# Optimization experiments

Hardware: AMD Instinct MI355X
Metric: run time of the kernel (lower is better)

Reference implementation:

```python
import jax, jax.numpy as jnp
import numpy as np
import math

D_MODEL = 1024
NUM_HEADS = 16
HEAD_DIM = D_MODEL // NUM_HEADS
EPS = 1e-6
ROPE_BASE = 10000.0


def _rope_cos_sin(seq_len, dim, dtype):
    inv_freq = 1.0 / (ROPE_BASE ** (jnp.arange(0, dim, 2, dtype=jnp.float32) / dim))
    t = jnp.arange(seq_len, dtype=jnp.float32)
    freqs = jnp.outer(t, inv_freq)                 # [s, dim/2]
    emb = jnp.concatenate([freqs, freqs], axis=-1)  # [s, dim]
    return jnp.cos(emb).astype(dtype), jnp.sin(emb).astype(dtype)


def _rotate_half(x):
    x1, x2 = jnp.split(x, 2, axis=-1)
    return jnp.concatenate([-x2, x1], axis=-1)


def setup_inputs() -> dict:
    key = jax.random.key(0)
    k1, k2, k3 = jax.random.split(key, 3)
    b, s = 2, 2048
    x = jax.random.normal(k1, (b, s, D_MODEL), dtype=jnp.float32)
    norm_w = jnp.ones((D_MODEL,), dtype=jnp.float32)
    qkv_w = jax.random.normal(k2, (3 * D_MODEL, D_MODEL), dtype=jnp.float32) * (1.0 / math.sqrt(D_MODEL))
    qkv_b = jnp.zeros((3 * D_MODEL,), dtype=jnp.float32)
    proj_w = jax.random.normal(k3, (D_MODEL, D_MODEL), dtype=jnp.float32) * (1.0 / math.sqrt(D_MODEL))
    proj_b = jnp.zeros((D_MODEL,), dtype=jnp.float32)
    return {"x": x, "norm_w": norm_w, "qkv_w": qkv_w, "qkv_b": qkv_b,
            "proj_w": proj_w, "proj_b": proj_b}


def reference(x, norm_w, qkv_w, qkv_b, proj_w, proj_b):
    b, s, d = x.shape
    # RMSNorm (pre-LN)
    xn = x * jax.lax.rsqrt(jnp.mean(x * x, axis=-1, keepdims=True) + EPS) * norm_w
    # Fused QKV
    qkv = jnp.einsum('bsd,ed->bse', xn, qkv_w) + qkv_b
    q, k, v = jnp.split(qkv, 3, axis=-1)
    # [b, h, s, hd]
    def shape(t):
        return t.reshape(b, s, NUM_HEADS, HEAD_DIM).transpose(0, 2, 1, 3)
    q, k, v = shape(q), shape(k), shape(v)
    # RoPE on head_dim
    cos, sin = _rope_cos_sin(s, HEAD_DIM, x.dtype)  # [s, hd]
    q = q * cos + _rotate_half(q) * sin
    k = k * cos + _rotate_half(k) * sin
    # Naive causal attention
    scale = 1.0 / math.sqrt(HEAD_DIM)
    scores = jnp.einsum('bhqd,bhkd->bhqk', q, k) * scale
    causal = jnp.tril(jnp.ones((s, s), dtype=bool))
    scores = jnp.where(causal, scores, -jnp.inf)
    attn = jax.nn.softmax(scores, axis=-1)
    y = jnp.einsum('bhqk,bhkd->bhqd', attn, v)
    y = y.transpose(0, 2, 1, 3).reshape(b, s, d)
    return jnp.einsum('bsd,ed->bse', y, proj_w) + proj_b
```

## Files before the change

kernel.cpp:

```cpp
#include <hip/hip_runtime.h>
#include <cstdint>
#include <cstddef>

#define NB 2
#define NS 2048
#define ND 1024
#define NH 16
#define HD 64
#define ROWS 4096
#define E3 3072

using bf16 = __bf16;
typedef __attribute__((ext_vector_type(4))) __bf16 bf16x4;
typedef __attribute__((ext_vector_type(8))) __bf16 bf16x8;
typedef __attribute__((ext_vector_type(4))) float f32x4;

__device__ __forceinline__ f32x4 mfma16(bf16x8 a, bf16x8 b, f32x4 c) {
    return __builtin_amdgcn_mfma_f32_16x16x32_bf16(a, b, c, 0, 0, 0);
}

__device__ __forceinline__ void gll16(const bf16* src, bf16* lds) {
    __builtin_amdgcn_global_load_lds(
        (const __attribute__((address_space(1))) void*)src,
        (__attribute__((address_space(3))) void*)lds, 16, 0, 0);
}

__global__ __launch_bounds__(256) void prep(const float* __restrict__ qkv_w,
                                            const float* __restrict__ proj_w,
                                            const float* __restrict__ x,
                                            const float* __restrict__ norm_w,
                                            bf16* __restrict__ wq,
                                            bf16* __restrict__ xn,
                                            float4* __restrict__ tab) {
    __shared__ float wsum[4];
    int bid = blockIdx.x;
    int tid = threadIdx.x;
    if (bid < 4096) {
        const int n1 = E3 * ND;
        int i = (bid * 256 + tid) * 4;
        const float* src = (i < n1) ? (qkv_w + i) : (proj_w + (i - n1));
        float4 v = *(const float4*)src;
        bf16x4 o;
        o[0] = (bf16)v.x; o[1] = (bf16)v.y; o[2] = (bf16)v.z; o[3] = (bf16)v.w;
        *(bf16x4*)(wq + i) = o;
    } else if (bid < 8192) {
        int row = bid - 4096;
        const float* xr = x + (size_t)row * ND;
        float4 v = ((const float4*)xr)[tid];
        float ss = v.x*v.x + v.y*v.y + v.z*v.z + v.w*v.w;
        #pragma unroll
        for (int m = 32; m >= 1; m >>= 1) ss += __shfl_xor(ss, m);
        if ((tid & 63) == 0) wsum[tid >> 6] = ss;
        __syncthreads();
        float total = wsum[0] + wsum[1] + wsum[2] + wsum[3];
        float scale = rsqrtf(total * (1.0f / ND) + 1e-6f);
        float4 wv = ((const float4*)norm_w)[tid];
        bf16x4 o;
        o[0] = (bf16)(v.x * scale * wv.x);
        o[1] = (bf16)(v.y * scale * wv.y);
        o[2] = (bf16)(v.z * scale * wv.z);
        o[3] = (bf16)(v.w * scale * wv.w);
        ((bf16x4*)(xn + (size_t)row * ND))[tid] = o;
    } else {
        int idx = (bid - 8192) * 256 + tid;
        int s = idx >> 4, j = idx & 15;
        float f0 = powf(10000.0f, -(float)j * (1.0f / 32.0f));
        float f1 = powf(10000.0f, -(float)(j + 16) * (1.0f / 32.0f));
        float sn0, c0, sn1, c1;
        sincosf((float)s * f0, &sn0, &c0);
        sincosf((float)s * f1, &sn1, &c1);
        tab[idx] = make_float4(c0, sn0, c1, sn1);
    }
}

__global__ __launch_bounds__(256) void gemm_qkv_rope(const bf16* __restrict__ A,
                                                     const bf16* __restrict__ Bm,
                                                     const float* __restrict__ bias,
                                                     const float4* __restrict__ tab,
                                                     bf16* __restrict__ Qb,
                                                     bf16* __restrict__ Kb,
                                                     bf16* __restrict__ Vf) {
    const int K = ND;
    __shared__ bf16 smem[8192];
    bf16* Asm = smem;
    bf16* Bsm = smem + 4096;
    const int tid = threadIdx.x;
    const int wave = tid >> 6, lane = tid & 63;
    const int quad = lane >> 4, l15 = lane & 15;
    const int row0 = blockIdx.x * 128, col0 = blockIdx.y * 128;
    const int wr = (wave >> 1) * 64, wc = (wave & 1) * 64;
    const int srow = lane >> 2;
    const int scol = (lane & 3) * 8;

    f32x4 acc[4][4] = {};

    for (int k0 = 0; k0 < K; k0 += 32) {
        #pragma unroll
        for (int i = 0; i < 2; ++i) {
            int r = wave * 32 + i * 16;
            gll16(A + (size_t)(row0 + r + srow) * K + k0 + scol, Asm + r * 32);
            gll16(Bm + (size_t)(col0 + r + srow) * K + k0 + scol, Bsm + r * 32);
        }
        __syncthreads();
        bf16x8 af[4], bff[4];
        #pragma unroll
        for (int t = 0; t < 4; ++t) {
            af[t]  = *(const bf16x8*)(Asm + (wr + t * 16 + l15) * 32 + quad * 8);
            bff[t] = *(const bf16x8*)(Bsm + (wc + t * 16 + l15) * 32 + quad * 8);
        }
        #pragma unroll
        for (int mt = 0; mt < 4; ++mt)
            #pragma unroll
            for (int nt = 0; nt < 4; ++nt)
                acc[mt][nt] = mfma16(af[mt], bff[nt], acc[mt][nt]);
        __syncthreads();
    }

    float bb[4];
    #pragma unroll
    for (int nt = 0; nt < 4; ++nt) bb[nt] = bias[col0 + wc + nt * 16 + l15];

    const int region = col0 >> 10;
    if (region == 2) {
        const int cv = col0 - 2048 + wc;
        const int h = cv >> 6;
        const int b = row0 >> 11;
        const int sloc = row0 & (NS - 1);
        const int kg0 = (sloc + wr) >> 5;
        bf16* vh = Vf + (size_t)(b * NH + h) * 131072;
        #pragma unroll
        for (int Gw = 0; Gw < 2; ++Gw) {
            #pragma unroll
            for (int nt = 0; nt < 4; ++nt) {
                bf16x8 vf8;
                #pragma unroll
                for (int r = 0; r < 4; ++r) {
                    vf8[r]     = (bf16)(acc[2 * Gw][nt][r] + bb[nt]);
                    vf8[4 + r] = (bf16)(acc[2 * Gw + 1][nt][r] + bb[nt]);
                }
                *(bf16x8*)(vh + ((size_t)(kg0 + Gw) * 4 + nt) * 512 + lane * 8) = vf8;
            }
        }
    } else {
        const float scale = (region == 0) ? 0.125f : 1.0f;
        bf16* Ob = (region == 0) ? Qb : Kb;
        const int h = ((col0 + wc) & 1023) >> 6;
        bf16* ep = smem + wave * 2048;
        #pragma unroll
        for (int p = 0; p < 2; ++p) {
            #pragma unroll
            for (int mtl = 0; mtl < 2; ++mtl) {
                const int mt = p * 2 + mtl;
                #pragma unroll
                for (int r = 0; r < 4; ++r) {
                    int row = row0 + wr + mt * 16 + quad * 4 + r;
                    int s = row & (NS - 1);
                    float4 cs = tab[s * 16 + l15];
                    #pragma unroll
                    for (int nt = 0; nt < 4; ++nt) {
                        float v  = acc[mt][nt][r] + bb[nt];
                        float vp = acc[mt][nt ^ 2][r] + bb[nt ^ 2];
                        float cc = (nt & 1) ? cs.z : cs.x;
                        float ss = (nt & 1) ? cs.w : cs.y;
                        float res = (nt < 2) ? (v * cc - vp * ss) : (v * cc + vp * ss);
                        ep[(mtl * 16 + quad * 4 + r) * 64 + nt * 16 + l15] = (bf16)(res * scale);
                    }
                }
            }
            asm volatile("s_waitcnt lgkmcnt(0)" ::: "memory");
            const int rowp = row0 + wr + p * 32;
            const int b = rowp >> 11;
            const int s0p = rowp & (NS - 1);
            bf16* gbase = Ob + ((size_t)(b * NH + h) * NS + s0p + (lane >> 3)) * 64 + (lane & 7) * 8;
            const bf16* lbase = ep + (lane >> 3) * 64 + (lane & 7) * 8;
            #pragma unroll
            for (int i = 0; i < 4; ++i) {
                bf16x8 v8 = *(const bf16x8*)(lbase + i * 512);
                *(bf16x8*)(gbase + (size_t)i * 512) = v8;
            }
            asm volatile("s_waitcnt lgkmcnt(0)" ::: "memory");
        }
    }
}

__global__ __launch_bounds__(256) void gemm_proj(const bf16* __restrict__ A,
                                                 const bf16* __restrict__ Bm,
                                                 const float* __restrict__ bias,
                                                 float* __restrict__ C) {
    __shared__ bf16 Asm[128 * 32];
    __shared__ bf16 Bsm[64 * 32];
    const int tid = threadIdx.x;
    const int wave = tid >> 6, lane = tid & 63;
    const int quad = lane >> 4, l15 = lane & 15;
    const int row0 = blockIdx.x * 128, col0 = blockIdx.y * 64;
    const int wr = (wave >> 1) * 64, wc = (wave & 1) * 32;
    const int srow = lane >> 2;
    const int scol = (lane & 3) * 8;

    f32x4 acc[4][2] = {};

    for (int k0 = 0; k0 < ND; k0 += 32) {
        gll16(A + (size_t)(row0 + wave * 32 + srow) * ND + k0 + scol, Asm + (wave * 32) * 32);
        gll16(A + (size_t)(row0 + wave * 32 + 16 + srow) * ND + k0 + scol, Asm + (wave * 32 + 16) * 32);
        gll16(Bm + (size_t)(col0 + wave * 16 + srow) * ND + k0 + scol, Bsm + (wave * 16) * 32);
        __syncthreads();
        bf16x8 af[4], bff[2];
        #pragma unroll
        for (int t = 0; t < 4; ++t)
            af[t] = *(const bf16x8*)(Asm + (wr + t * 16 + l15) * 32 + quad * 8);
        #pragma unroll
        for (int t = 0; t < 2; ++t)
            bff[t] = *(const bf16x8*)(Bsm + (wc + t * 16 + l15) * 32 + quad * 8);
        #pragma unroll
        for (int mt = 0; mt < 4; ++mt)
            #pragma unroll
            for (int nt = 0; nt < 2; ++nt)
                acc[mt][nt] = mfma16(af[mt], bff[nt], acc[mt][nt]);
        __syncthreads();
    }

    #pragma unroll
    for (int nt = 0; nt < 2; ++nt) {
        int col = col0 + wc + nt * 16 + l15;
        float bv = bias[col];
        #pragma unroll
        for (int mt = 0; mt < 4; ++mt) {
            int row = row0 + wr + mt * 16 + quad * 4;
            #pragma unroll
            for (int r = 0; r < 4; ++r)
                C[(size_t)(row + r) * ND + col] = acc[mt][nt][r] + bv;
        }
    }
}

__global__ __launch_bounds__(256) void attn(const bf16* __restrict__ Q,
                                            const bf16* __restrict__ K,
                                            const bf16* __restrict__ Vf,
                                            bf16* __restrict__ Y) {
    __shared__ bf16 Ksm[2][8192];
    __shared__ bf16 Vsm[2][8192];
    int bid = blockIdx.x;
    int g = bid >> 5;
    int bh = bid & 31;
    int qt = (g < 8) ? (15 - g) : (g - 8);
    int tid = threadIdx.x;
    int wave = tid >> 6, lane = tid & 63;
    int quad = lane >> 4, l15 = lane & 15;
    int q0 = qt * 128 + wave * 32;
    const bf16* Qh = Q + (size_t)bh * NS * 64;
    const bf16* Kh = K + (size_t)bh * NS * 64;
    const float NEG_INF = -__builtin_inff();

    const int krow = wave * 8 + (lane >> 3);
    const int ksx  = (lane & 7) ^ (krow & 7);
    const bf16* sK = Kh + (size_t)krow * 64 + ksx * 8;
    const bf16* sV = Vf + (size_t)bh * 131072 + wave * 2048 + lane * 8;

    const bf16* pk0 = &Ksm[0][l15 * 64 + ((quad) ^ (l15 & 7)) * 8];
    const bf16* pk1 = &Ksm[0][l15 * 64 + ((4 + quad) ^ (l15 & 7)) * 8];
    const bf16* pvf = &Vsm[0][lane * 8];

    bf16x8 bq[2][2];
    #pragma unroll
    for (int t = 0; t < 2; ++t)
        #pragma unroll
        for (int hh = 0; hh < 2; ++hh)
            bq[t][hh] = *(const bf16x8*)(Qh + (size_t)(q0 + t * 16 + l15) * 64 + hh * 32 + quad * 8);

    f32x4 o[2][4] = {};
    float lsum[2] = {0.f, 0.f};

    auto stage = [&](int c, int par) {
        const int kb = c * 128;
        bf16* dK = &Ksm[par][wave * 512];
        bf16* dV = &Vsm[par][wave * 2048];
        #pragma unroll
        for (int i = 0; i < 4; ++i)
            gll16(sK + (size_t)(kb + i * 32) * 64, dK + i * 2048);
        #pragma unroll
        for (int nt = 0; nt < 4; ++nt)
            gll16(sV + (size_t)(kb >> 5) * 2048 + nt * 512, dV + nt * 512);
    };

    auto compute = [&](int cc, int par) {
        const int kb = cc * 128;
        const int pb = par * 8192;
        #pragma unroll
        for (int ksub = 0; ksub < 4; ++ksub) {
            const int kbs = kb + ksub * 32;
            if (kbs <= q0) {
                bf16x8 ak00 = *(const bf16x8*)(pk0 + pb + ksub * 2048);
                bf16x8 ak01 = *(const bf16x8*)(pk1 + pb + ksub * 2048);
                bf16x8 ak10 = *(const bf16x8*)(pk0 + pb + ksub * 2048 + 1024);
                bf16x8 ak11 = *(const bf16x8*)(pk1 + pb + ksub * 2048 + 1024);
                bf16x8 vf0 = *(const bf16x8*)(pvf + pb + ksub * 2048);
                bf16x8 vf1 = *(const bf16x8*)(pvf + pb + ksub * 2048 + 512);
                bf16x8 vf2 = *(const bf16x8*)(pvf + pb + ksub * 2048 + 1024);
                bf16x8 vf3 = *(const bf16x8*)(pvf + pb + ksub * 2048 + 1536);
                const bool masked = (kbs == q0);
                #pragma unroll
                for (int t = 0; t < 2; ++t) {
                    f32x4 sh0 = {}, sh1 = {};
                    sh0 = mfma16(ak00, bq[t][0], sh0);
                    sh0 = mfma16(ak01, bq[t][1], sh0);
                    sh1 = mfma16(ak10, bq[t][0], sh1);
                    sh1 = mfma16(ak11, bq[t][1], sh1);
                    if (masked) {
                        int qy = q0 + t * 16 + l15;
                        #pragma unroll
                        for (int r = 0; r < 4; ++r) {
                            if (kbs + quad * 4 + r > qy)      sh0[r] = NEG_INF;
                            if (kbs + 16 + quad * 4 + r > qy) sh1[r] = NEG_INF;
                        }
                    }
                    bf16x8 pa;
                    float ls = 0.f;
                    #pragma unroll
                    for (int j = 0; j < 4; ++j) {
                        float p0 = __expf(sh0[j]);
                        float p1 = __expf(sh1[j]);
                        ls += p0 + p1;
                        pa[j] = (bf16)p0;
                        pa[4 + j] = (bf16)p1;
                    }
                    lsum[t] += ls;
                    o[t][0] = mfma16(pa, vf0, o[t][0]);
                    o[t][1] = mfma16(pa, vf1, o[t][1]);
                    o[t][2] = mfma16(pa, vf2, o[t][2]);
                    o[t][3] = mfma16(pa, vf3, o[t][3]);
                }
            }
        }
    };

    const int ncb = qt + 1;
    stage(0, 0);
    __syncthreads();
    for (int c = 0; c < ncb; ++c) {
        const int par = c & 1;
        if (c + 1 < ncb) stage(c + 1, par ^ 1);
        compute(c, par);
        __syncthreads();
    }

    int b = bh >> 4, h = bh & 15;
    bf16* ep = &Ksm[0][wave * 2048];
    #pragma unroll
    for (int t = 0; t < 2; ++t) {
        float red = lsum[t];
        red += __shfl_xor(red, 16);
        red += __shfl_xor(red, 32);
        #pragma unroll
        for (int r = 0; r < 4; ++r) {
            float il = 1.0f / __shfl(red, quad * 4 + r);
            #pragma unroll
            for (int nt = 0; nt < 4; ++nt)
                ep[(t * 16 + quad * 4 + r) * 64 + nt * 16 + l15] = (bf16)(o[t][nt][r] * il);
        }
    }
    asm volatile("s_waitcnt lgkmcnt(0)" ::: "memory");
    bf16* gbase = Y + ((size_t)(b * NS + q0 + (lane >> 3)) << 10) + h * 64 + (lane & 7) * 8;
    const bf16* lbase = ep + (lane >> 3) * 64 + (lane & 7) * 8;
    #pragma unroll
    for (int i = 0; i < 4; ++i) {
        bf16x8 v8 = *(const bf16x8*)(lbase + i * 512);
        *(bf16x8*)(gbase + ((size_t)i * 8 << 10)) = v8;
    }
}

extern "C" void kernel_launch(void* const* d_in, const int* in_sizes, int n_in,
                              void* d_out, int out_size, void* d_ws, size_t ws_size,
                              hipStream_t stream) {
    const float* x      = (const float*)d_in[0];
    const float* norm_w = (const float*)d_in[1];
    const float* qkv_w  = (const float*)d_in[2];
    const float* qkv_b  = (const float*)d_in[3];
    const float* proj_w = (const float*)d_in[4];
    const float* proj_b = (const float*)d_in[5];
    float* out = (float*)d_out;

    char* ws = (char*)d_ws;
    size_t off = 0;
    bf16* xn    = (bf16*)(ws + off); off += (size_t)ROWS * ND * 2;
    bf16* wq    = (bf16*)(ws + off); off += (size_t)E3 * ND * 2;
    bf16* wp    = (bf16*)(ws + off); off += (size_t)ND * ND * 2;
    bf16* Qb    = (bf16*)(ws + off); off += (size_t)NB * NH * NS * HD * 2;
    bf16* Kb    = (bf16*)(ws + off); off += (size_t)NB * NH * NS * HD * 2;
    bf16* Vfrag = (bf16*)(ws + off); off += (size_t)NB * NH * HD * NS * 2;
    bf16* Y     = (bf16*)(ws + off); off += (size_t)ROWS * ND * 2;
    float4* tab = (float4*)(ws + off); off += (size_t)NS * 16 * sizeof(float4);

    prep<<<8320, 256, 0, stream>>>(qkv_w, proj_w, x, norm_w, wq, xn, tab);
    gemm_qkv_rope<<<dim3(ROWS / 128, E3 / 128), 256, 0, stream>>>(xn, wq, qkv_b, tab, Qb, Kb, Vfrag);
    attn<<<NB * NH * (NS / 128), 256, 0, stream>>>(Qb, Kb, Vfrag, Y);
    gemm_proj<<<dim3(ROWS / 128, ND / 64), 256, 0, stream>>>(Y, wp, proj_b, out);
}
```

Baseline: 189.4 us.

## Double GEMM K-tile to 64 with XOR-swizzled LDS layout in QKV and proj

Both the QKV+RoPE GEMM and the output projection GEMM now stage 64-wide K slices per iteration instead of 32, halving the number of barrier pairs and global-load issue rounds. The LDS tile is stored with an XOR swizzle of the 16-byte column chunk by row, so that fragment reads across 16 lanes avoid bank conflicts. The cost is doubled LDS per block, which may reduce occupancy. The attention kernel is untouched, so the gain is limited to the GEMM stages.

```diff
diff --git a/kernel.cpp b/kernel.cpp
--- a/kernel.cpp
+++ b/kernel.cpp
@@ -81,38 +81,44 @@
                                                      bf16* __restrict__ Kb,
                                                      bf16* __restrict__ Vf) {
     const int K = ND;
-    __shared__ bf16 smem[8192];
+    __shared__ bf16 smem[16384];
     bf16* Asm = smem;
-    bf16* Bsm = smem + 4096;
+    bf16* Bsm = smem + 8192;
     const int tid = threadIdx.x;
     const int wave = tid >> 6, lane = tid & 63;
     const int quad = lane >> 4, l15 = lane & 15;
     const int row0 = blockIdx.x * 128, col0 = blockIdx.y * 128;
     const int wr = (wave >> 1) * 64, wc = (wave & 1) * 64;
-    const int srow = lane >> 2;
-    const int scol = (lane & 3) * 8;
+    const int x7 = l15 & 7;
+
+    const int sR = lane >> 3;
+    const int sC = (lane & 7) ^ sR;
+    const bf16* sA = A + (size_t)(row0 + wave * 8 + sR) * K + sC * 8;
+    const bf16* sB = Bm + (size_t)(col0 + wave * 8 + sR) * K + sC * 8;
 
     f32x4 acc[4][4] = {};
 
-    for (int k0 = 0; k0 < K; k0 += 32) {
-        #pragma unroll
-        for (int i = 0; i < 2; ++i) {
-            int r = wave * 32 + i * 16;
-            gll16(A + (size_t)(row0 + r + srow) * K + k0 + scol, Asm + r * 32);
-            gll16(Bm + (size_t)(col0 + r + srow) * K + k0 + scol, Bsm + r * 32);
-        }
-        __syncthreads();
-        bf16x8 af[4], bff[4];
-        #pragma unroll
-        for (int t = 0; t < 4; ++t) {
-            af[t]  = *(const bf16x8*)(Asm + (wr + t * 16 + l15) * 32 + quad * 8);
-            bff[t] = *(const bf16x8*)(Bsm + (wc + t * 16 + l15) * 32 + quad * 8);
-        }
-        #pragma unroll
-        for (int mt = 0; mt < 4; ++mt)
-            #pragma unroll
-            for (int nt = 0; nt < 4; ++nt)
-                acc[mt][nt] = mfma16(af[mt], bff[nt], acc[mt][nt]);
+    for (int k0 = 0; k0 < K; k0 += 64) {
+        #pragma unroll
+        for (int i = 0; i < 4; ++i) {
+            gll16(sA + (size_t)(i * 32) * K + k0, Asm + (i * 32 + wave * 8) * 64);
+            gll16(sB + (size_t)(i * 32) * K + k0, Bsm + (i * 32 + wave * 8) * 64);
+        }
+        __syncthreads();
+        #pragma unroll
+        for (int kk = 0; kk < 2; ++kk) {
+            bf16x8 af[4], bff[4];
+            #pragma unroll
+            for (int t = 0; t < 4; ++t) {
+                af[t]  = *(const bf16x8*)(Asm + (wr + t * 16 + l15) * 64 + (((kk * 4 + quad) ^ x7) * 8));
+                bff[t] = *(const bf16x8*)(Bsm + (wc + t * 16 + l15) * 64 + (((kk * 4 + quad) ^ x7) * 8));
+            }
+            #pragma unroll
+            for (int mt = 0; mt < 4; ++mt)
+                #pragma unroll
+                for (int nt = 0; nt < 4; ++nt)
+                    acc[mt][nt] = mfma16(af[mt], bff[nt], acc[mt][nt]);
+        }
         __syncthreads();
     }
 
@@ -187,35 +193,45 @@
                                                  const bf16* __restrict__ Bm,
                                                  const float* __restrict__ bias,
                                                  float* __restrict__ C) {
-    __shared__ bf16 Asm[128 * 32];
-    __shared__ bf16 Bsm[64 * 32];
+    __shared__ bf16 Asm[8192];
+    __shared__ bf16 Bsm[4096];
     const int tid = threadIdx.x;
     const int wave = tid >> 6, lane = tid & 63;
     const int quad = lane >> 4, l15 = lane & 15;
     const int row0 = blockIdx.x * 128, col0 = blockIdx.y * 64;
     const int wr = (wave >> 1) * 64, wc = (wave & 1) * 32;
-    const int srow = lane >> 2;
-    const int scol = (lane & 3) * 8;
+    const int x7 = l15 & 7;
+
+    const int sR = lane >> 3;
+    const int sC = (lane & 7) ^ sR;
+    const bf16* sA = A + (size_t)(row0 + wave * 8 + sR) * ND + sC * 8;
+    const bf16* sB = Bm + (size_t)(col0 + wave * 8 + sR) * ND + sC * 8;
 
     f32x4 acc[4][2] = {};
 
-    for (int k0 = 0; k0 < ND; k0 += 32) {
-        gll16(A + (size_t)(row0 + wave * 32 + srow) * ND + k0 + scol, Asm + (wave * 32) * 32);
-        gll16(A + (size_t)(row0 + wave * 32 + 16 + srow) * ND + k0 + scol, Asm + (wave * 32 + 16) * 32);
-        gll16(Bm + (size_t)(col0 + wave * 16 + srow) * ND + k0 + scol, Bsm + (wave * 16) * 32);
-        __syncthreads();
-        bf16x8 af[4], bff[2];
-        #pragma unroll
-        for (int t = 0; t < 4; ++t)
-            af[t] = *(const bf16x8*)(Asm + (wr + t * 16 + l15) * 32 + quad * 8);
-        #pragma unroll
-        for (int t = 0; t < 2; ++t)
-            bff[t] = *(const bf16x8*)(Bsm + (wc + t * 16 + l15) * 32 + quad * 8);
-        #pragma unroll
-        for (int mt = 0; mt < 4; ++mt)
-            #pragma unroll
-            for (int nt = 0; nt < 2; ++nt)
-                acc[mt][nt] = mfma16(af[mt], bff[nt], acc[mt][nt]);
+    for (int k0 = 0; k0 < ND; k0 += 64) {
+        #pragma unroll
+        for (int i = 0; i < 4; ++i)
+            gll16(sA + (size_t)(i * 32) * ND + k0, Asm + (i * 32 + wave * 8) * 64);
+        #pragma unroll
+        for (int i = 0; i < 2; ++i)
+            gll16(sB + (size_t)(i * 32) * ND + k0, Bsm + (i * 32 + wave * 8) * 64);
+        __syncthreads();
+        #pragma unroll
+        for (int kk = 0; kk < 2; ++kk) {
+            bf16x8 af[4], bff[2];
+            #pragma unroll
+            for (int t = 0; t < 4; ++t)
+                af[t] = *(const bf16x8*)(Asm + (wr + t * 16 + l15) * 64 + (((kk * 4 + quad) ^ x7) * 8));
+            #pragma unroll
+            for (int t = 0; t < 2; ++t)
+                bff[t] = *(const bf16x8*)(Bsm + (wc + t * 16 + l15) * 64 + (((kk * 4 + quad) ^ x7) * 8));
+            #pragma unroll
+            for (int mt = 0; mt < 4; ++mt)
+                #pragma unroll
+                for (int nt = 0; nt < 2; ++nt)
+                    acc[mt][nt] = mfma16(af[mt], bff[nt], acc[mt][nt]);
+        }
         __syncthreads();
     }
 
```

Result: slower. 196.0 us (+3.5%).
